# Performance work log

Measured on AMD Instinct MI355X. Metric: run time of the kernel, lower is better.

The kernel has to match this reference:

```python
import jax, jax.numpy as jnp
import numpy as np

N = 100000      # nodes
E = 1600000     # edges (avg degree 16)
F_IN = 128      # num_features
H = 64          # hidden_dim
C = 7           # num_classes


def setup_inputs() -> dict:
    key = jax.random.key(0)
    ks = jax.random.split(key, 9)
    x = jax.random.normal(ks[0], (N, F_IN), dtype=jnp.float32)
    edge_index = jax.random.randint(ks[1], (2, E), 0, N, dtype=jnp.int32)
    s1 = 1.0 / np.sqrt(F_IN)
    s2 = 1.0 / np.sqrt(H)
    # SAGEConv1: lin_l applied to aggregated neighbors, lin_r to root
    W1l = jax.random.uniform(ks[2], (F_IN, H), jnp.float32, -s1, s1)
    W1r = jax.random.uniform(ks[3], (F_IN, H), jnp.float32, -s1, s1)
    b1 = jax.random.uniform(ks[4], (H,), jnp.float32, -s1, s1)
    # SAGEConv2
    W2l = jax.random.uniform(ks[5], (H, C), jnp.float32, -s2, s2)
    W2r = jax.random.uniform(ks[6], (H, C), jnp.float32, -s2, s2)
    b2 = jax.random.uniform(ks[7], (C,), jnp.float32, -s2, s2)
    return {"x": x, "edge_index": edge_index, "W1l": W1l, "W1r": W1r,
            "b1": b1, "W2l": W2l, "W2r": W2r, "b2": b2}


def _segment_mean(vals, idx, num_segments):
    # scatter-mean: sum messages per destination node, divide by in-degree
    sums = jax.ops.segment_sum(vals, idx, num_segments=num_segments)
    cnt = jax.ops.segment_sum(jnp.ones(idx.shape, vals.dtype), idx,
                              num_segments=num_segments)
    return sums / jnp.maximum(cnt, 1.0)[:, None]


def reference(x, edge_index, W1l, W1r, b1, W2l, W2r, b2):
    src, dst = edge_index[0], edge_index[1]
    # SAGEConv 1: mean of neighbor (src) features at each dst, plus root term
    agg1 = _segment_mean(x[src], dst, N)              # [N, F_IN]
    h = agg1 @ W1l + x @ W1r + b1                     # [N, H]
    h = jax.nn.relu(h)
    # dropout is inactive in eval mode (deterministic reference)
    # SAGEConv 2
    agg2 = _segment_mean(h[src], dst, N)              # [N, H]
    out = agg2 @ W2l + h @ W2r + b2                   # [N, C]
    return jax.nn.log_softmax(out, axis=1)
```

## Files before the change

### kernel.cpp

```cpp
#include <hip/hip_runtime.h>
#include <cstdint>
#include <cstddef>


#define CAP 64
#define BINSZ 128
#define CH 4096

typedef __attribute__((ext_vector_type(8))) short bf16x8v;
typedef __attribute__((ext_vector_type(4))) float f32x4v;

__device__ __forceinline__ float bf2f(unsigned short u) {
  return __uint_as_float(((unsigned int)u) << 16);
}
__device__ __forceinline__ unsigned short f2bf(float f) {
  unsigned int x = __float_as_uint(f);
  unsigned int r = (x + 0x7fffu + ((x >> 16) & 1u)) >> 16;
  return (unsigned short)r;
}

__global__ __launch_bounds__(256) void k_hist(const int* __restrict__ ei,
                                              int* __restrict__ hist,
                                              const float* __restrict__ W1l,
                                              const float* __restrict__ W1r,
                                              unsigned short* __restrict__ wswz,
                                              int E, int NB, int NCH) {
  const int t = threadIdx.x;
  if (blockIdx.x >= (unsigned)NCH) {
    int idx = (blockIdx.x - NCH) * 256 + t;
    int j = idx & 7;
    int lane = (idx >> 3) & 63;
    int c = (idx >> 9) & 7;
    int t4 = idx >> 12;
    int kk = t4 * 32 + (lane >> 4) * 8 + j;
    int nn = c * 16 + (lane & 15);
    float v = (nn < 64) ? W1l[kk * 64 + nn] : W1r[kk * 64 + (nn - 64)];
    wswz[idx] = f2bf(v);
    return;
  }
  __shared__ int lcnt[1024];
  const int c = blockIdx.x;
  for (int i = t; i < NB; i += 256) lcnt[i] = 0;
  __syncthreads();
  const int base = c * CH;
  const int end = min(base + CH, E);
  for (int e = base + t; e < end; e += 256) {
    int d = ei[E + e];
    atomicAdd(&lcnt[d >> 7], 1);
  }
  __syncthreads();
  for (int i = t; i < NB; i += 256) hist[(size_t)i * NCH + c] = lcnt[i];
}

__global__ __launch_bounds__(256) void k_scan_gemm(
    int* __restrict__ hist, int* __restrict__ tot, int NB, int NCH, int nScan,
    const float* __restrict__ x, const unsigned short* __restrict__ wswz,
    const float* __restrict__ b1, unsigned short* __restrict__ xl,
    unsigned short* __restrict__ hroot, int Nn) {
  if (blockIdx.x < (unsigned)nScan) {
    const int lane = threadIdx.x & 63;
    const int bin = blockIdx.x * 4 + (threadIdx.x >> 6);
    if (bin >= NB) return;
    int* h = hist + (size_t)bin * NCH;
    int carry = 0;
    for (int base = 0; base < NCH; base += 64) {
      int i = base + lane;
      int v = (i < NCH) ? h[i] : 0;
      int incl = v;
      #pragma unroll
      for (int d = 1; d < 64; d <<= 1) {
        int t = __shfl_up(incl, d, 64);
        if (lane >= d) incl += t;
      }
      if (i < NCH) h[i] = carry + incl - v;
      carry += __shfl(incl, 63, 64);
    }
    if (lane == 0) tot[bin] = carry;
    return;
  }
  __shared__ unsigned short Bsw[16384];
  const int t = threadIdx.x;
  const int bid = blockIdx.x - nScan;
  {
    const uint4* src = (const uint4*)wswz;
    uint4* dst = (uint4*)Bsw;
    #pragma unroll
    for (int i = 0; i < 8; ++i) dst[t + i * 256] = src[t + i * 256];
  }
  __syncthreads();

  const int lane = t & 63;
  const int wid = t >> 6;
  const int quad = lane >> 4;
  const int m = lane & 15;
  const int rowA = bid * 64 + wid * 16 + m;
  const float* xrow = x + (size_t)min(rowA, Nn - 1) * 128;

  f32x4v acc[8];
  #pragma unroll
  for (int c = 0; c < 8; ++c) acc[c] = (f32x4v){0.f, 0.f, 0.f, 0.f};

  #pragma unroll
  for (int t4 = 0; t4 < 4; ++t4) {
    const int koff = t4 * 32 + quad * 8;
    float4 a0 = *(const float4*)(xrow + koff);
    float4 a1 = *(const float4*)(xrow + koff + 4);
    bf16x8v af;
    af[0] = (short)f2bf(a0.x); af[1] = (short)f2bf(a0.y);
    af[2] = (short)f2bf(a0.z); af[3] = (short)f2bf(a0.w);
    af[4] = (short)f2bf(a1.x); af[5] = (short)f2bf(a1.y);
    af[6] = (short)f2bf(a1.z); af[7] = (short)f2bf(a1.w);
    #pragma unroll
    for (int c = 0; c < 8; ++c) {
      const bf16x8v bf_ = *(const bf16x8v*)&Bsw[(((t4 * 8 + c) * 64 + lane)) << 3];
      acc[c] = __builtin_amdgcn_mfma_f32_16x16x32_bf16(af, bf_, acc[c], 0, 0, 0);
    }
  }

  const int rbase = bid * 64 + wid * 16 + quad * 4;
  #pragma unroll
  for (int c = 0; c < 8; ++c) {
    const int col = c * 16 + m;
    #pragma unroll
    for (int i = 0; i < 4; ++i) {
      const int r = rbase + i;
      if (r < Nn) {
        if (c < 4) xl[(size_t)r * 64 + col] = f2bf(acc[c][i]);
        else       hroot[(size_t)r * 64 + (col - 64)] = f2bf(acc[c][i] + b1[col - 64]);
      }
    }
  }
}

__global__ __launch_bounds__(64) void k_scanB(const int* __restrict__ tot,
                                              int* __restrict__ binbase, int NB) {
  const int lane = threadIdx.x;
  int carry = 0;
  for (int base = 0; base < NB; base += 64) {
    int i = base + lane;
    int v = (i < NB) ? tot[i] : 0;
    int incl = v;
    #pragma unroll
    for (int d = 1; d < 64; d <<= 1) {
      int t = __shfl_up(incl, d, 64);
      if (lane >= d) incl += t;
    }
    if (i < NB) binbase[i] = carry + incl - v;
    carry += __shfl(incl, 63, 64);
  }
  if (lane == 0) binbase[NB] = carry;
}

__global__ __launch_bounds__(256) void k_scat(const int* __restrict__ ei,
                                              const int* __restrict__ hist,
                                              const int* __restrict__ binbase,
                                              unsigned int* __restrict__ part,
                                              int E, int NB, int NCH) {
  __shared__ int lcur[1024];
  const int c = blockIdx.x, t = threadIdx.x;
  for (int i = t; i < NB; i += 256)
    lcur[i] = hist[(size_t)i * NCH + c] + binbase[i];
  __syncthreads();
  const int base = c * CH;
  const int end = min(base + CH, E);
  for (int e = base + t; e < end; e += 256) {
    int s = ei[e];
    int d = ei[E + e];
    int bin = d >> 7;
    int pos = atomicAdd(&lcur[bin], 1);
    part[pos] = (unsigned)s | ((unsigned)(d & 127) << 17);
  }
}

__global__ __launch_bounds__(256) void k_bucketB(const int* __restrict__ binbase,
                                                 const unsigned int* __restrict__ part,
                                                 int* __restrict__ cnt,
                                                 int* __restrict__ bucket) {
  __shared__ int lbkt[BINSZ * CAP];
  __shared__ int ldeg[BINSZ];
  const int b = blockIdx.x, t = threadIdx.x;
  if (t < BINSZ) ldeg[t] = 0;
  __syncthreads();
  const int e0 = binbase[b], e1 = binbase[b + 1];
  for (int i = e0 + t; i < e1; i += 256) {
    unsigned rec = part[i];
    int loc = rec >> 17;
    int p = atomicAdd(&ldeg[loc], 1);
    if (p < CAP) lbkt[loc * CAP + p] = (int)(rec & 0x1FFFFu);
  }
  __syncthreads();
  if (t < BINSZ) cnt[b * BINSZ + t] = ldeg[t];
  const int4* s4 = (const int4*)lbkt;
  int4* d4 = (int4*)(bucket + (size_t)b * BINSZ * CAP);
  #pragma unroll 2
  for (int i = t; i < BINSZ * CAP / 4; i += 256) d4[i] = s4[i];
}

__global__ __launch_bounds__(256) void k_agg1(
    const int* __restrict__ cnt, const int* __restrict__ bucket,
    const unsigned int* __restrict__ xl32, const unsigned int* __restrict__ hroot32,
    unsigned int* __restrict__ hbuf32, int Nn) {
  const int lane = threadIdx.x & 63;
  const int q = lane & 15;
  const int g = lane >> 4;
  const int nw = gridDim.x * (blockDim.x >> 6);
  int n = blockIdx.x * (blockDim.x >> 6) + (threadIdx.x >> 6);
  if (n >= Nn) return;

  int c  = cnt[n];
  int c1 = cnt[min(n + nw, Nn - 1)];
  int m = c < CAP ? c : CAP;
  int sidx = (lane < m) ? bucket[(size_t)n * CAP + lane] : 0;
  if ((unsigned)sidx >= (unsigned)Nn) sidx = 0;
  uint2 hu = *(const uint2*)(hroot32 + (size_t)n * 32 + 2 * q);

  while (true) {
    const int n1 = n + nw;
    const int n1c = min(n1, Nn - 1);
    const int m1 = c1 < CAP ? c1 : CAP;
    int sidx1 = (lane < m1) ? bucket[(size_t)n1c * CAP + lane] : 0;
    uint2 hu1 = *(const uint2*)(hroot32 + (size_t)n1c * 32 + 2 * q);
    int c2 = cnt[min(n1 + nw, Nn - 1)];

    float a0 = 0.f, a1 = 0.f, a2 = 0.f, a3 = 0.f;
    int i = 0;
    for (; i + 16 <= m; i += 16) {
      int rA = __shfl(sidx, i + g, 64);
      int rB = __shfl(sidx, i + 4 + g, 64);
      int rC = __shfl(sidx, i + 8 + g, 64);
      int rD = __shfl(sidx, i + 12 + g, 64);
      uint2 uA = *(const uint2*)(xl32 + (size_t)rA * 32 + 2 * q);
      uint2 uB = *(const uint2*)(xl32 + (size_t)rB * 32 + 2 * q);
      uint2 uC = *(const uint2*)(xl32 + (size_t)rC * 32 + 2 * q);
      uint2 uD = *(const uint2*)(xl32 + (size_t)rD * 32 + 2 * q);
      a0 += (__uint_as_float(uA.x << 16) + __uint_as_float(uB.x << 16))
          + (__uint_as_float(uC.x << 16) + __uint_as_float(uD.x << 16));
      a1 += (__uint_as_float(uA.x & 0xFFFF0000u) + __uint_as_float(uB.x & 0xFFFF0000u))
          + (__uint_as_float(uC.x & 0xFFFF0000u) + __uint_as_float(uD.x & 0xFFFF0000u));
      a2 += (__uint_as_float(uA.y << 16) + __uint_as_float(uB.y << 16))
          + (__uint_as_float(uC.y << 16) + __uint_as_float(uD.y << 16));
      a3 += (__uint_as_float(uA.y & 0xFFFF0000u) + __uint_as_float(uB.y & 0xFFFF0000u))
          + (__uint_as_float(uC.y & 0xFFFF0000u) + __uint_as_float(uD.y & 0xFFFF0000u));
    }
    for (; i + 8 <= m; i += 8) {
      int rA = __shfl(sidx, i + g, 64);
      int rB = __shfl(sidx, i + 4 + g, 64);
      uint2 uA = *(const uint2*)(xl32 + (size_t)rA * 32 + 2 * q);
      uint2 uB = *(const uint2*)(xl32 + (size_t)rB * 32 + 2 * q);
      a0 += __uint_as_float(uA.x << 16) + __uint_as_float(uB.x << 16);
      a1 += __uint_as_float(uA.x & 0xFFFF0000u) + __uint_as_float(uB.x & 0xFFFF0000u);
      a2 += __uint_as_float(uA.y << 16) + __uint_as_float(uB.y << 16);
      a3 += __uint_as_float(uA.y & 0xFFFF0000u) + __uint_as_float(uB.y & 0xFFFF0000u);
    }
    for (; i < m; i += 4) {
      int e = i + g;
      int r = __shfl(sidx, e & 63, 64);
      uint2 u = *(const uint2*)(xl32 + (size_t)r * 32 + 2 * q);
      if (e < m) {
        a0 += __uint_as_float(u.x << 16);
        a1 += __uint_as_float(u.x & 0xFFFF0000u);
        a2 += __uint_as_float(u.y << 16);
        a3 += __uint_as_float(u.y & 0xFFFF0000u);
      }
    }
    a0 += __shfl_xor(a0, 16, 64); a0 += __shfl_xor(a0, 32, 64);
    a1 += __shfl_xor(a1, 16, 64); a1 += __shfl_xor(a1, 32, 64);
    a2 += __shfl_xor(a2, 16, 64); a2 += __shfl_xor(a2, 32, 64);
    a3 += __shfl_xor(a3, 16, 64); a3 += __shfl_xor(a3, 32, 64);
    if (g == 0) {
      float dd = c > 0 ? (float)c : 1.f;
      float h0 = fmaxf(a0 / dd + __uint_as_float(hu.x << 16), 0.f);
      float h1 = fmaxf(a1 / dd + __uint_as_float(hu.x & 0xFFFF0000u), 0.f);
      float h2 = fmaxf(a2 / dd + __uint_as_float(hu.y << 16), 0.f);
      float h3 = fmaxf(a3 / dd + __uint_as_float(hu.y & 0xFFFF0000u), 0.f);
      uint2 o;
      o.x = (unsigned)f2bf(h0) | ((unsigned)f2bf(h1) << 16);
      o.y = (unsigned)f2bf(h2) | ((unsigned)f2bf(h3) << 16);
      *(uint2*)(hbuf32 + (size_t)n * 32 + 2 * q) = o;
    }
    if (n1 >= Nn) break;
    n = n1; c = c1; c1 = c2; m = m1;
    sidx = ((unsigned)sidx1 >= (unsigned)Nn) ? 0 : sidx1;
    hu = hu1;
  }
}

__global__ __launch_bounds__(128) void k_gemm2(
    const unsigned short* __restrict__ hbuf,
    const float* __restrict__ W2l, const float* __restrict__ W2r,
    const float* __restrict__ b2,
    float* __restrict__ hl, float* __restrict__ hr, int Nn) {
  __shared__ float tile[128 * 65];
  const int t = threadIdx.x;
  const int rowbase = blockIdx.x * 128;
  for (int idx = t; idx < 128 * 64; idx += 128) {
    int r = idx >> 6, k = idx & 63;
    int n = rowbase + r;
    tile[r * 65 + k] = (n < Nn) ? bf2f(hbuf[(size_t)n * 64 + k]) : 0.f;
  }
  __syncthreads();
  int n = rowbase + t;
  if (n >= Nn) return;
  float al[7] = {0, 0, 0, 0, 0, 0, 0};
  float ar[7] = {0, 0, 0, 0, 0, 0, 0};
  for (int k = 0; k < 64; ++k) {
    float hv = tile[t * 65 + k];
    #pragma unroll
    for (int c = 0; c < 7; ++c) {
      al[c] = fmaf(hv, W2l[k * 7 + c], al[c]);
      ar[c] = fmaf(hv, W2r[k * 7 + c], ar[c]);
    }
  }
  #pragma unroll
  for (int c = 0; c < 7; ++c) {
    hl[(size_t)n * 8 + c] = al[c];
    hr[(size_t)n * 8 + c] = ar[c] + b2[c];
  }
  hl[(size_t)n * 8 + 7] = 0.f;
  hr[(size_t)n * 8 + 7] = 0.f;
}

__global__ __launch_bounds__(256) void k_out(
    const int* __restrict__ cnt, const int* __restrict__ bucket,
    const float* __restrict__ hl, const float* __restrict__ hr,
    float* __restrict__ out, int Nn) {
  const int lane = threadIdx.x & 63;
  const int c = lane & 7;
  const int sub = lane >> 3;
  const int gw = blockIdx.x * (blockDim.x >> 6) + (threadIdx.x >> 6);
  const int n = gw * 8 + sub;
  if (n >= Nn) return;
  int cn = cnt[n];
  int m = cn < CAP ? cn : CAP;
  const bool act = (c < 7);
  float acc = 0.f;
  for (int e0 = 0; e0 < m; e0 += 8) {
    int bv = (e0 + c < m) ? bucket[(size_t)n * CAP + e0 + c] : 0;
    #pragma unroll
    for (int cc = 0; cc < 8; ++cc) {
      if (e0 + cc < m) {
        int s = __shfl(bv, (lane & 56) + cc, 64);
        if ((unsigned)s >= (unsigned)Nn) s = 0;
        if (act) acc += hl[(size_t)s * 8 + c];
      }
    }
  }
  float dd = cn > 0 ? (float)cn : 1.f;
  float v = act ? (acc / dd + hr[(size_t)n * 8 + c]) : -INFINITY;
  float mx = v;
  mx = fmaxf(mx, __shfl_xor(mx, 1, 8));
  mx = fmaxf(mx, __shfl_xor(mx, 2, 8));
  mx = fmaxf(mx, __shfl_xor(mx, 4, 8));
  float ex = act ? expf(v - mx) : 0.f;
  float s2 = ex;
  s2 += __shfl_xor(s2, 1, 8);
  s2 += __shfl_xor(s2, 2, 8);
  s2 += __shfl_xor(s2, 4, 8);
  float res = v - mx - logf(s2);
  if (act) out[(size_t)n * 7 + c] = res;
}

static inline size_t alignup(size_t v) { return (v + 255) & ~(size_t)255; }

extern "C" void kernel_launch(void* const* d_in, const int* in_sizes, int n_in,
                              void* d_out, int out_size, void* d_ws, size_t ws_size,
                              hipStream_t stream) {
  const int N = in_sizes[0] / 128;
  const int E = in_sizes[1] / 2;
  const int NB = (N + BINSZ - 1) / BINSZ;
  const int Np = NB * BINSZ;
  const int NCH = (E + CH - 1) / CH;
  const int nScan = (NB + 3) / 4;

  const float* x   = (const float*)d_in[0];
  const int*   ei  = (const int*)d_in[1];
  const float* W1l = (const float*)d_in[2];
  const float* W1r = (const float*)d_in[3];
  const float* b1  = (const float*)d_in[4];
  const float* W2l = (const float*)d_in[5];
  const float* W2r = (const float*)d_in[6];
  const float* b2  = (const float*)d_in[7];
  float* out = (float*)d_out;

  char* p = (char*)d_ws;
  int* hist    = (int*)p;            p += alignup((size_t)NB * NCH * 4);
  int* tot     = (int*)p;            p += alignup((size_t)NB * 4);
  int* binbase = (int*)p;            p += alignup((size_t)(NB + 1) * 4);
  unsigned int* part = (unsigned int*)p; p += alignup((size_t)E * 4);
  int* cnt    = (int*)p;             p += alignup((size_t)Np * 4);
  int* bucket = (int*)p;             p += alignup((size_t)Np * CAP * 4);
  unsigned short* wswz = (unsigned short*)p; p += alignup((size_t)16384 * 2);
  unsigned short* xl    = (unsigned short*)p; p += alignup((size_t)N * 64 * 2);
  unsigned short* hroot = (unsigned short*)p; p += alignup((size_t)N * 64 * 2);
  unsigned short* hbuf  = (unsigned short*)p; p += alignup((size_t)N * 64 * 2);
  float* hl  = (float*)p;            p += alignup((size_t)N * 8 * 4);
  float* hr  = (float*)p;            p += alignup((size_t)N * 8 * 4);

  dim3 b256(256);
  k_hist<<<dim3(NCH + 64), b256, 0, stream>>>(ei, hist, W1l, W1r, wswz, E, NB, NCH);
  k_scan_gemm<<<dim3(nScan + (N + 63) / 64), b256, 0, stream>>>(
      hist, tot, NB, NCH, nScan, x, wswz, b1, xl, hroot, N);
  k_scanB<<<dim3(1), dim3(64), 0, stream>>>(tot, binbase, NB);
  k_scat<<<dim3(NCH), b256, 0, stream>>>(ei, hist, binbase, part, E, NB, NCH);
  k_bucketB<<<dim3(NB), b256, 0, stream>>>(binbase, part, cnt, bucket);
  k_agg1<<<dim3(2048), b256, 0, stream>>>(cnt, bucket,
      (const unsigned int*)xl, (const unsigned int*)hroot, (unsigned int*)hbuf, N);
  k_gemm2<<<dim3((N + 127) / 128), dim3(128), 0, stream>>>(hbuf, W2l, W2r, b2, hl, hr, N);
  const int waves_out = (N + 7) / 8;
  k_out<<<dim3((waves_out + 3) / 4), b256, 0, stream>>>(cnt, bucket, hl, hr, out, N);
}
```

Before: 241.9 us.

## Aggregate directly from binned edge partitions with LDS float atomics, drop bucket pass

Removes the per-node bucket build kernel and the single-block bin scan. Bin base offsets now come from an atomic cursor in the scan kernel, which orders bins arbitrarily but keeps them contiguous. Both aggregation kernels process one 128-node bin per block, reading the partitioned edge records and accumulating neighbour features into shared memory with float atomicAdd, then normalise by the counted degree. This saves the bucket write and read traffic and two launches, and removes the 64-neighbour cap. The cost is heavy LDS atomic contention and a nondeterministic summation order.

```diff
diff --git a/kernel.cpp b/kernel.cpp
--- a/kernel.cpp
+++ b/kernel.cpp
@@ -3,7 +3,6 @@
 #include <cstddef>
 
 
-#define CAP 64
 #define BINSZ 128
 #define CH 4096
 
@@ -24,9 +23,11 @@
                                               const float* __restrict__ W1l,
                                               const float* __restrict__ W1r,
                                               unsigned short* __restrict__ wswz,
+                                              int* __restrict__ cursor,
                                               int E, int NB, int NCH) {
   const int t = threadIdx.x;
   if (blockIdx.x >= (unsigned)NCH) {
+    if (blockIdx.x == (unsigned)NCH && t == 0) *cursor = 0;
     int idx = (blockIdx.x - NCH) * 256 + t;
     int j = idx & 7;
     int lane = (idx >> 3) & 63;
@@ -53,7 +54,8 @@
 }
 
 __global__ __launch_bounds__(256) void k_scan_gemm(
-    int* __restrict__ hist, int* __restrict__ tot, int NB, int NCH, int nScan,
+    int* __restrict__ hist, int* __restrict__ tot, int* __restrict__ binbase,
+    int* __restrict__ cursor, int NB, int NCH, int nScan,
     const float* __restrict__ x, const unsigned short* __restrict__ wswz,
     const float* __restrict__ b1, unsigned short* __restrict__ xl,
     unsigned short* __restrict__ hroot, int Nn) {
@@ -75,7 +77,10 @@
       if (i < NCH) h[i] = carry + incl - v;
       carry += __shfl(incl, 63, 64);
     }
-    if (lane == 0) tot[bin] = carry;
+    if (lane == 0) {
+      tot[bin] = carry;
+      binbase[bin] = atomicAdd(cursor, carry);
+    }
     return;
   }
   __shared__ unsigned short Bsw[16384];
@@ -132,25 +137,6 @@
   }
 }
 
-__global__ __launch_bounds__(64) void k_scanB(const int* __restrict__ tot,
-                                              int* __restrict__ binbase, int NB) {
-  const int lane = threadIdx.x;
-  int carry = 0;
-  for (int base = 0; base < NB; base += 64) {
-    int i = base + lane;
-    int v = (i < NB) ? tot[i] : 0;
-    int incl = v;
-    #pragma unroll
-    for (int d = 1; d < 64; d <<= 1) {
-      int t = __shfl_up(incl, d, 64);
-      if (lane >= d) incl += t;
-    }
-    if (i < NB) binbase[i] = carry + incl - v;
-    carry += __shfl(incl, 63, 64);
-  }
-  if (lane == 0) binbase[NB] = carry;
-}
-
 __global__ __launch_bounds__(256) void k_scat(const int* __restrict__ ei,
                                               const int* __restrict__ hist,
                                               const int* __restrict__ binbase,
@@ -172,116 +158,73 @@
   }
 }
 
-__global__ __launch_bounds__(256) void k_bucketB(const int* __restrict__ binbase,
-                                                 const unsigned int* __restrict__ part,
-                                                 int* __restrict__ cnt,
-                                                 int* __restrict__ bucket) {
-  __shared__ int lbkt[BINSZ * CAP];
-  __shared__ int ldeg[BINSZ];
-  const int b = blockIdx.x, t = threadIdx.x;
-  if (t < BINSZ) ldeg[t] = 0;
-  __syncthreads();
-  const int e0 = binbase[b], e1 = binbase[b + 1];
-  for (int i = e0 + t; i < e1; i += 256) {
-    unsigned rec = part[i];
-    int loc = rec >> 17;
-    int p = atomicAdd(&ldeg[loc], 1);
-    if (p < CAP) lbkt[loc * CAP + p] = (int)(rec & 0x1FFFFu);
-  }
-  __syncthreads();
-  if (t < BINSZ) cnt[b * BINSZ + t] = ldeg[t];
-  const int4* s4 = (const int4*)lbkt;
-  int4* d4 = (int4*)(bucket + (size_t)b * BINSZ * CAP);
-  #pragma unroll 2
-  for (int i = t; i < BINSZ * CAP / 4; i += 256) d4[i] = s4[i];
-}
-
-__global__ __launch_bounds__(256) void k_agg1(
-    const int* __restrict__ cnt, const int* __restrict__ bucket,
+__global__ __launch_bounds__(512) void k_agg1(
+    const unsigned int* __restrict__ part,
+    const int* __restrict__ binbase, const int* __restrict__ tot,
     const unsigned int* __restrict__ xl32, const unsigned int* __restrict__ hroot32,
     unsigned int* __restrict__ hbuf32, int Nn) {
-  const int lane = threadIdx.x & 63;
-  const int q = lane & 15;
-  const int g = lane >> 4;
-  const int nw = gridDim.x * (blockDim.x >> 6);
-  int n = blockIdx.x * (blockDim.x >> 6) + (threadIdx.x >> 6);
-  if (n >= Nn) return;
-
-  int c  = cnt[n];
-  int c1 = cnt[min(n + nw, Nn - 1)];
-  int m = c < CAP ? c : CAP;
-  int sidx = (lane < m) ? bucket[(size_t)n * CAP + lane] : 0;
-  if ((unsigned)sidx >= (unsigned)Nn) sidx = 0;
-  uint2 hu = *(const uint2*)(hroot32 + (size_t)n * 32 + 2 * q);
-
-  while (true) {
-    const int n1 = n + nw;
-    const int n1c = min(n1, Nn - 1);
-    const int m1 = c1 < CAP ? c1 : CAP;
-    int sidx1 = (lane < m1) ? bucket[(size_t)n1c * CAP + lane] : 0;
-    uint2 hu1 = *(const uint2*)(hroot32 + (size_t)n1c * 32 + 2 * q);
-    int c2 = cnt[min(n1 + nw, Nn - 1)];
-
-    float a0 = 0.f, a1 = 0.f, a2 = 0.f, a3 = 0.f;
-    int i = 0;
-    for (; i + 16 <= m; i += 16) {
-      int rA = __shfl(sidx, i + g, 64);
-      int rB = __shfl(sidx, i + 4 + g, 64);
-      int rC = __shfl(sidx, i + 8 + g, 64);
-      int rD = __shfl(sidx, i + 12 + g, 64);
-      uint2 uA = *(const uint2*)(xl32 + (size_t)rA * 32 + 2 * q);
-      uint2 uB = *(const uint2*)(xl32 + (size_t)rB * 32 + 2 * q);
-      uint2 uC = *(const uint2*)(xl32 + (size_t)rC * 32 + 2 * q);
-      uint2 uD = *(const uint2*)(xl32 + (size_t)rD * 32 + 2 * q);
-      a0 += (__uint_as_float(uA.x << 16) + __uint_as_float(uB.x << 16))
-          + (__uint_as_float(uC.x << 16) + __uint_as_float(uD.x << 16));
-      a1 += (__uint_as_float(uA.x & 0xFFFF0000u) + __uint_as_float(uB.x & 0xFFFF0000u))
-          + (__uint_as_float(uC.x & 0xFFFF0000u) + __uint_as_float(uD.x & 0xFFFF0000u));
-      a2 += (__uint_as_float(uA.y << 16) + __uint_as_float(uB.y << 16))
-          + (__uint_as_float(uC.y << 16) + __uint_as_float(uD.y << 16));
-      a3 += (__uint_as_float(uA.y & 0xFFFF0000u) + __uint_as_float(uB.y & 0xFFFF0000u))
-          + (__uint_as_float(uC.y & 0xFFFF0000u) + __uint_as_float(uD.y & 0xFFFF0000u));
-    }
-    for (; i + 8 <= m; i += 8) {
-      int rA = __shfl(sidx, i + g, 64);
-      int rB = __shfl(sidx, i + 4 + g, 64);
-      uint2 uA = *(const uint2*)(xl32 + (size_t)rA * 32 + 2 * q);
-      uint2 uB = *(const uint2*)(xl32 + (size_t)rB * 32 + 2 * q);
-      a0 += __uint_as_float(uA.x << 16) + __uint_as_float(uB.x << 16);
-      a1 += __uint_as_float(uA.x & 0xFFFF0000u) + __uint_as_float(uB.x & 0xFFFF0000u);
-      a2 += __uint_as_float(uA.y << 16) + __uint_as_float(uB.y << 16);
-      a3 += __uint_as_float(uA.y & 0xFFFF0000u) + __uint_as_float(uB.y & 0xFFFF0000u);
-    }
-    for (; i < m; i += 4) {
-      int e = i + g;
-      int r = __shfl(sidx, e & 63, 64);
-      uint2 u = *(const uint2*)(xl32 + (size_t)r * 32 + 2 * q);
-      if (e < m) {
-        a0 += __uint_as_float(u.x << 16);
-        a1 += __uint_as_float(u.x & 0xFFFF0000u);
-        a2 += __uint_as_float(u.y << 16);
-        a3 += __uint_as_float(u.y & 0xFFFF0000u);
-      }
-    }
-    a0 += __shfl_xor(a0, 16, 64); a0 += __shfl_xor(a0, 32, 64);
-    a1 += __shfl_xor(a1, 16, 64); a1 += __shfl_xor(a1, 32, 64);
-    a2 += __shfl_xor(a2, 16, 64); a2 += __shfl_xor(a2, 32, 64);
-    a3 += __shfl_xor(a3, 16, 64); a3 += __shfl_xor(a3, 32, 64);
-    if (g == 0) {
-      float dd = c > 0 ? (float)c : 1.f;
-      float h0 = fmaxf(a0 / dd + __uint_as_float(hu.x << 16), 0.f);
-      float h1 = fmaxf(a1 / dd + __uint_as_float(hu.x & 0xFFFF0000u), 0.f);
-      float h2 = fmaxf(a2 / dd + __uint_as_float(hu.y << 16), 0.f);
-      float h3 = fmaxf(a3 / dd + __uint_as_float(hu.y & 0xFFFF0000u), 0.f);
-      uint2 o;
-      o.x = (unsigned)f2bf(h0) | ((unsigned)f2bf(h1) << 16);
-      o.y = (unsigned)f2bf(h2) | ((unsigned)f2bf(h3) << 16);
-      *(uint2*)(hbuf32 + (size_t)n * 32 + 2 * q) = o;
-    }
-    if (n1 >= Nn) break;
-    n = n1; c = c1; c1 = c2; m = m1;
-    sidx = ((unsigned)sidx1 >= (unsigned)Nn) ? 0 : sidx1;
-    hu = hu1;
+  __shared__ float accS[128 * 65];
+  __shared__ int degS[128];
+  const int t = threadIdx.x;
+  const int b = blockIdx.x;
+  for (int i = t; i < 128 * 65; i += 512) accS[i] = 0.f;
+  if (t < 128) degS[t] = 0;
+  __syncthreads();
+
+  const int e0 = binbase[b];
+  const int e1 = e0 + tot[b];
+  const int q = t & 15;
+  const int gid = t >> 4;
+  const int qo = 2 * q;
+
+  for (int base = e0; base < e1; base += 64) {
+    const int eA = base + gid;
+    const int eB = base + 32 + gid;
+    const bool vA = eA < e1, vB = eB < e1;
+    unsigned recA = vA ? part[eA] : 0u;
+    unsigned recB = vB ? part[eB] : 0u;
+    int sA = min((int)(recA & 0x1FFFFu), Nn - 1);
+    int sB = min((int)(recB & 0x1FFFFu), Nn - 1);
+    uint2 uA = *(const uint2*)(xl32 + (unsigned)sA * 32 + qo);
+    uint2 uB = *(const uint2*)(xl32 + (unsigned)sB * 32 + qo);
+    const int locA = (int)(recA >> 17), locB = (int)(recB >> 17);
+    if (vA) {
+      float* a = &accS[locA * 65 + 4 * q];
+      atomicAdd(a + 0, __uint_as_float(uA.x << 16));
+      atomicAdd(a + 1, __uint_as_float(uA.x & 0xFFFF0000u));
+      atomicAdd(a + 2, __uint_as_float(uA.y << 16));
+      atomicAdd(a + 3, __uint_as_float(uA.y & 0xFFFF0000u));
+      if (q == 0) atomicAdd(&degS[locA], 1);
+    }
+    if (vB) {
+      float* a = &accS[locB * 65 + 4 * q];
+      atomicAdd(a + 0, __uint_as_float(uB.x << 16));
+      atomicAdd(a + 1, __uint_as_float(uB.x & 0xFFFF0000u));
+      atomicAdd(a + 2, __uint_as_float(uB.y << 16));
+      atomicAdd(a + 3, __uint_as_float(uB.y & 0xFFFF0000u));
+      if (q == 0) atomicAdd(&degS[locB], 1);
+    }
+  }
+  __syncthreads();
+
+  const int r = t >> 2, ch = t & 3;
+  const int n = b * 128 + r;
+  if (n < Nn) {
+    const int dg = degS[r];
+    const float inv = (dg > 0) ? __builtin_amdgcn_rcpf((float)dg) : 1.f;
+    const float* a = &accS[r * 65 + ch * 16];
+    uint4 h0 = *(const uint4*)(hroot32 + (size_t)n * 32 + ch * 8);
+    uint4 h1 = *(const uint4*)(hroot32 + (size_t)n * 32 + ch * 8 + 4);
+    const unsigned hu[8] = {h0.x, h0.y, h0.z, h0.w, h1.x, h1.y, h1.z, h1.w};
+    unsigned o[8];
+    #pragma unroll
+    for (int k = 0; k < 8; ++k) {
+      float lo = fmaxf(fmaf(a[2 * k],     inv, __uint_as_float(hu[k] << 16)), 0.f);
+      float hi = fmaxf(fmaf(a[2 * k + 1], inv, __uint_as_float(hu[k] & 0xFFFF0000u)), 0.f);
+      o[k] = (unsigned)f2bf(lo) | ((unsigned)f2bf(hi) << 16);
+    }
+    *(uint4*)(hbuf32 + (size_t)n * 32 + ch * 8)     = make_uint4(o[0], o[1], o[2], o[3]);
+    *(uint4*)(hbuf32 + (size_t)n * 32 + ch * 8 + 4) = make_uint4(o[4], o[5], o[6], o[7]);
   }
 }
 
@@ -320,44 +263,65 @@
   hr[(size_t)n * 8 + 7] = 0.f;
 }
 
-__global__ __launch_bounds__(256) void k_out(
-    const int* __restrict__ cnt, const int* __restrict__ bucket,
+__global__ __launch_bounds__(512) void k_out(
+    const unsigned int* __restrict__ part,
+    const int* __restrict__ binbase, const int* __restrict__ tot,
     const float* __restrict__ hl, const float* __restrict__ hr,
     float* __restrict__ out, int Nn) {
-  const int lane = threadIdx.x & 63;
-  const int c = lane & 7;
-  const int sub = lane >> 3;
-  const int gw = blockIdx.x * (blockDim.x >> 6) + (threadIdx.x >> 6);
-  const int n = gw * 8 + sub;
-  if (n >= Nn) return;
-  int cn = cnt[n];
-  int m = cn < CAP ? cn : CAP;
-  const bool act = (c < 7);
-  float acc = 0.f;
-  for (int e0 = 0; e0 < m; e0 += 8) {
-    int bv = (e0 + c < m) ? bucket[(size_t)n * CAP + e0 + c] : 0;
-    #pragma unroll
-    for (int cc = 0; cc < 8; ++cc) {
-      if (e0 + cc < m) {
-        int s = __shfl(bv, (lane & 56) + cc, 64);
-        if ((unsigned)s >= (unsigned)Nn) s = 0;
-        if (act) acc += hl[(size_t)s * 8 + c];
+  __shared__ float accS[128 * 9];
+  __shared__ int degS[128];
+  const int t = threadIdx.x;
+  const int b = blockIdx.x;
+  for (int i = t; i < 128 * 9; i += 512) accS[i] = 0.f;
+  if (t < 128) degS[t] = 0;
+  __syncthreads();
+
+  const int e0 = binbase[b];
+  const int e1 = e0 + tot[b];
+  const int c = t & 7;
+  const int gid = t >> 3;
+  for (int base = e0; base < e1; base += 128) {
+    const int eA = base + gid;
+    const int eB = base + 64 + gid;
+    const bool vA = eA < e1, vB = eB < e1;
+    unsigned recA = vA ? part[eA] : 0u;
+    unsigned recB = vB ? part[eB] : 0u;
+    int sA = min((int)(recA & 0x1FFFFu), Nn - 1);
+    int sB = min((int)(recB & 0x1FFFFu), Nn - 1);
+    float fA = hl[(size_t)sA * 8 + c];
+    float fB = hl[(size_t)sB * 8 + c];
+    const int locA = (int)(recA >> 17), locB = (int)(recB >> 17);
+    if (vA) {
+      atomicAdd(&accS[locA * 9 + c], fA);
+      if (c == 0) atomicAdd(&degS[locA], 1);
+    }
+    if (vB) {
+      atomicAdd(&accS[locB * 9 + c], fB);
+      if (c == 0) atomicAdd(&degS[locB], 1);
+    }
+  }
+  __syncthreads();
+
+  if (t < 128) {
+    const int n = b * 128 + t;
+    if (n < Nn) {
+      const int dg = degS[t];
+      const float inv = (dg > 0) ? 1.f / (float)dg : 1.f;
+      float v[7];
+      float mx = -INFINITY;
+      #pragma unroll
+      for (int cc = 0; cc < 7; ++cc) {
+        v[cc] = accS[t * 9 + cc] * inv + hr[(size_t)n * 8 + cc];
+        mx = fmaxf(mx, v[cc]);
       }
-    }
-  }
-  float dd = cn > 0 ? (float)cn : 1.f;
-  float v = act ? (acc / dd + hr[(size_t)n * 8 + c]) : -INFINITY;
-  float mx = v;
-  mx = fmaxf(mx, __shfl_xor(mx, 1, 8));
-  mx = fmaxf(mx, __shfl_xor(mx, 2, 8));
-  mx = fmaxf(mx, __shfl_xor(mx, 4, 8));
-  float ex = act ? expf(v - mx) : 0.f;
-  float s2 = ex;
-  s2 += __shfl_xor(s2, 1, 8);
-  s2 += __shfl_xor(s2, 2, 8);
-  s2 += __shfl_xor(s2, 4, 8);
-  float res = v - mx - logf(s2);
-  if (act) out[(size_t)n * 7 + c] = res;
+      float s2 = 0.f;
+      #pragma unroll
+      for (int cc = 0; cc < 7; ++cc) s2 += expf(v[cc] - mx);
+      const float ls = logf(s2);
+      #pragma unroll
+      for (int cc = 0; cc < 7; ++cc) out[(size_t)n * 7 + cc] = v[cc] - mx - ls;
+    }
+  }
 }
 
 static inline size_t alignup(size_t v) { return (v + 255) & ~(size_t)255; }
@@ -368,7 +332,6 @@
   const int N = in_sizes[0] / 128;
   const int E = in_sizes[1] / 2;
   const int NB = (N + BINSZ - 1) / BINSZ;
-  const int Np = NB * BINSZ;
   const int NCH = (E + CH - 1) / CH;
   const int nScan = (NB + 3) / 4;
 
@@ -386,9 +349,8 @@
   int* hist    = (int*)p;            p += alignup((size_t)NB * NCH * 4);
   int* tot     = (int*)p;            p += alignup((size_t)NB * 4);
   int* binbase = (int*)p;            p += alignup((size_t)(NB + 1) * 4);
+  int* cursor  = (int*)p;            p += alignup(4);
   unsigned int* part = (unsigned int*)p; p += alignup((size_t)E * 4);
-  int* cnt    = (int*)p;             p += alignup((size_t)Np * 4);
-  int* bucket = (int*)p;             p += alignup((size_t)Np * CAP * 4);
   unsigned short* wswz = (unsigned short*)p; p += alignup((size_t)16384 * 2);
   unsigned short* xl    = (unsigned short*)p; p += alignup((size_t)N * 64 * 2);
   unsigned short* hroot = (unsigned short*)p; p += alignup((size_t)N * 64 * 2);
@@ -396,16 +358,13 @@
   float* hl  = (float*)p;            p += alignup((size_t)N * 8 * 4);
   float* hr  = (float*)p;            p += alignup((size_t)N * 8 * 4);
 
-  dim3 b256(256);
-  k_hist<<<dim3(NCH + 64), b256, 0, stream>>>(ei, hist, W1l, W1r, wswz, E, NB, NCH);
+  dim3 b256(256), b512(512);
+  k_hist<<<dim3(NCH + 64), b256, 0, stream>>>(ei, hist, W1l, W1r, wswz, cursor, E, NB, NCH);
   k_scan_gemm<<<dim3(nScan + (N + 63) / 64), b256, 0, stream>>>(
-      hist, tot, NB, NCH, nScan, x, wswz, b1, xl, hroot, N);
-  k_scanB<<<dim3(1), dim3(64), 0, stream>>>(tot, binbase, NB);
+      hist, tot, binbase, cursor, NB, NCH, nScan, x, wswz, b1, xl, hroot, N);
   k_scat<<<dim3(NCH), b256, 0, stream>>>(ei, hist, binbase, part, E, NB, NCH);
-  k_bucketB<<<dim3(NB), b256, 0, stream>>>(binbase, part, cnt, bucket);
-  k_agg1<<<dim3(2048), b256, 0, stream>>>(cnt, bucket,
+  k_agg1<<<dim3(NB), b512, 0, stream>>>(part, binbase, tot,
       (const unsigned int*)xl, (const unsigned int*)hroot, (unsigned int*)hbuf, N);
   k_gemm2<<<dim3((N + 127) / 128), dim3(128), 0, stream>>>(hbuf, W2l, W2r, b2, hl, hr, N);
-  const int waves_out = (N + 7) / 8;
-  k_out<<<dim3((waves_out + 3) / 4), b256, 0, stream>>>(cnt, bucket, hl, hr, out, N);
-}
+  k_out<<<dim3(NB), b512, 0, stream>>>(part, binbase, tot, hl, hr, out, N);
+}
```

Measured after the change: 948.2 us. +292.0%, slower.
